# Kernel tuning notes

Hardware: AMD Instinct MI355X
Metric: run time of the kernel (lower is better)

The kernel has to match this reference:

```python
import jax, jax.numpy as jnp
import numpy as np

K = 3          # involution kernel size
GROUPS = 32    # channels == GROUPS * K*K
BN_EPS = 1e-5

def _conv1x1(x, W, b):
    # x: (B,C,H,W), W: (Co,C), b: (Co,)
    return jnp.einsum('bchw,oc->bohw', x, W) + b[None, :, None, None]

def setup_inputs() -> dict:
    key = jax.random.key(0)
    ks = jax.random.split(key, 5)
    C = GROUPS * K * K  # 288
    x = jax.random.normal(ks[0], (8, C, 64, 64), dtype=jnp.float32)
    Wi = jax.random.normal(ks[1], (C, C), dtype=jnp.float32) * 0.05
    bi = jnp.zeros((C,), dtype=jnp.float32)
    gamma = jnp.ones((C,), dtype=jnp.float32)
    beta = jnp.zeros((C,), dtype=jnp.float32)
    Wo = jax.random.normal(ks[2], (C, C), dtype=jnp.float32) * 0.05
    bo = jnp.zeros((C,), dtype=jnp.float32)
    return {"x": x, "Wi": Wi, "bi": bi, "gamma": gamma, "beta": beta, "Wo": Wo, "bo": bo}

def reference(x, Wi, bi, gamma, beta, Wo, bo):
    B, C, H, W = x.shape
    # kernel generation branch (stride=1 -> avgpool is identity)
    tmp = jax.nn.relu(_conv1x1(x, Wi, bi))
    # BatchNorm2d in training mode: batch stats over (N,H,W), biased variance
    mean = jnp.mean(tmp, axis=(0, 2, 3), keepdims=True)
    var = jnp.var(tmp, axis=(0, 2, 3), keepdims=True)
    tmp = (tmp - mean) * jax.lax.rsqrt(var + BN_EPS)
    tmp = tmp * gamma[None, :, None, None] + beta[None, :, None, None]
    ker = _conv1x1(tmp, Wo, bo)                       # (B, G*K^2, H, W)
    ker = ker.reshape(B, GROUPS, K * K, H, W)         # (B, G, K^2, H, W)
    # unfold: extract KxK patches with padding (K-1)//2, stride 1
    p = (K - 1) // 2
    xp = jnp.pad(x, ((0, 0), (0, 0), (p, p), (p, p)))
    patches = jnp.stack(
        [xp[:, :, i:i + H, j:j + W] for i in range(K) for j in range(K)],
        axis=2,
    )  # (B, C, K^2, H, W), kernel-position minor — matches torch unfold layout
    patches = patches.reshape(B, GROUPS, C // GROUPS, K * K, H, W)
    # per-pixel dynamic kernel multiply + sum over kernel positions
    out = jnp.einsum('bgkhw,bgckhw->bgchw', ker, patches)
    return out.reshape(B, C, H, W)
```

## Files before the change

kernel.cpp:

```cpp
#include <hip/hip_runtime.h>

#define CH   288
#define GRPS 32
#define CPG  9
#define IMH  64
#define IMW  64
#define HW   4096
#define NB   8
#define NPX  (NB * HW)
#define BN_EPS 1e-5f

typedef short bf16x8 __attribute__((ext_vector_type(8)));
typedef float f32x4  __attribute__((ext_vector_type(4)));

#define XT_OFF   0u
#define WIB_OFF  18874368u
#define WOS_OFF  19040256u
#define S1_OFF   19206144u
#define S2_OFF   19207296u
#define SC_OFF   19208448u
#define SH_OFF   19209600u
#define BO2_OFF  19210752u

__device__ __forceinline__ unsigned short f2b(float f) {
    unsigned int u = __float_as_uint(f);
    return (unsigned short)((u + 0x7fffu + ((u >> 16) & 1u)) >> 16);
}
__device__ __forceinline__ float b2f(unsigned short h) {
    return __uint_as_float(((unsigned int)h) << 16);
}

#define GLDS(g, l) __builtin_amdgcn_global_load_lds( \
    (const __attribute__((address_space(1))) void*)(g), \
    (__attribute__((address_space(3))) void*)(l), 16, 0, 0)

__device__ __forceinline__ f32x4 mfma16(bf16x8 a, bf16x8 b, f32x4 c) {
    return __builtin_amdgcn_mfma_f32_16x16x32_bf16(a, b, c, 0, 0, 0);
}

#define TS 40
__global__ __launch_bounds__(256) void k_transpose(const float* __restrict__ x,
                                                   unsigned short* __restrict__ xt) {
    __shared__ unsigned short T[64 * TS];
    const int tid = threadIdx.x;
    const int p0 = blockIdx.x * 64;
    const int c0 = blockIdx.y * 32;
    const int b  = blockIdx.z;
    #pragma unroll
    for (int it = 0; it < 2; ++it) {
        const int item  = it * 256 + tid;
        const int c_loc = item >> 4;
        const int p4    = item & 15;
        const float4 v = *(const float4*)(x + (size_t)(b * CH + c0 + c_loc) * HW + p0 + p4 * 4);
        const int px = p4 * 4;
        T[(px + 0) * TS + c_loc] = f2b(v.x);
        T[(px + 1) * TS + c_loc] = f2b(v.y);
        T[(px + 2) * TS + c_loc] = f2b(v.z);
        T[(px + 3) * TS + c_loc] = f2b(v.w);
    }
    __syncthreads();
    const int px_loc = tid >> 2;
    const int cq     = tid & 3;
    const uint4 o = *(const uint4*)((const char*)T + px_loc * (TS * 2) + cq * 16);
    *(uint4*)(xt + ((size_t)b * HW + p0 + px_loc) * CH + c0 + cq * 8) = o;
}

__global__ __launch_bounds__(256) void k_cvt_wi(const float* __restrict__ Wi,
                                                unsigned short* __restrict__ Wib) {
    const int idx = blockIdx.x * 256 + threadIdx.x;
    const float4 v = ((const float4*)Wi)[idx];
    unsigned short h[4] = {f2b(v.x), f2b(v.y), f2b(v.z), f2b(v.w)};
    *(uint2*)(Wib + (size_t)idx * 4) = *(const uint2*)h;
}

__global__ __launch_bounds__(256) void k_gemm1(const unsigned short* __restrict__ Wib,
                                               const float* __restrict__ bi,
                                               unsigned short* __restrict__ xt,
                                               float* __restrict__ s1g) {
    __shared__ unsigned short smem[(64 + 288) * 32];
    char* smc = (char*)smem;

    const int tid  = threadIdx.x;
    const int wave = tid >> 6;
    const int lane = tid & 63;
    const int q    = lane >> 4;
    const int r    = lane & 15;
    const int pxh  = wave & 1;
    const int chh  = wave >> 1;
    const int p0   = blockIdx.x * 64;

    f32x4 acc[2][9];
    #pragma unroll
    for (int t = 0; t < 2; ++t)
        #pragma unroll
        for (int j = 0; j < 9; ++j) acc[t][j] = (f32x4)0.0f;

    const int lrow = lane >> 2;
    const int lp   = lane & 3;

    for (int k0 = 0; k0 < CH; k0 += 32) {
        for (int s = wave; s < 22; s += 4) {
            const int row = s * 16 + lrow;
            const int sc  = lp ^ ((row >> 1) & 3);
            const unsigned short* g = (s < 4)
                ? xt  + (size_t)(p0 + row) * CH + k0 + sc * 8
                : Wib + (size_t)(row - 64) * CH + k0 + sc * 8;
            GLDS(g, smc + s * 1024);
        }
        __syncthreads();
        bf16x8 xf[2];
        #pragma unroll
        for (int t = 0; t < 2; ++t) {
            const int row = pxh * 32 + t * 16 + r;
            xf[t] = *(const bf16x8*)(smc + row * 64 + ((q ^ ((row >> 1) & 3)) * 16));
        }
        #pragma unroll
        for (int j = 0; j < 9; ++j) {
            const int ro = 64 + chh * 144 + j * 16 + r;
            const bf16x8 wf = *(const bf16x8*)(smc + ro * 64 + ((q ^ ((ro >> 1) & 3)) * 16));
            acc[0][j] = mfma16(wf, xf[0], acc[0][j]);
            acc[1][j] = mfma16(wf, xf[1], acc[1][j]);
        }
        __syncthreads();
    }

    float* sstat = (float*)(smc + 18432);
    for (int c2 = tid; c2 < 576; c2 += 256) sstat[c2] = 0.0f;
    __syncthreads();

    #pragma unroll 1
    for (int j = 0; j < 9; ++j) {
        const int cb = chh * 144 + j * 16 + q * 4;
        const float4 b4 = *(const float4*)(bi + cb);
        float a1[4] = {0.f, 0.f, 0.f, 0.f}, a2[4] = {0.f, 0.f, 0.f, 0.f};
        #pragma unroll
        for (int t = 0; t < 2; ++t) {
            float v0 = fmaxf(acc[t][j][0] + b4.x, 0.0f);
            float v1 = fmaxf(acc[t][j][1] + b4.y, 0.0f);
            float v2 = fmaxf(acc[t][j][2] + b4.z, 0.0f);
            float v3 = fmaxf(acc[t][j][3] + b4.w, 0.0f);
            a1[0] += v0; a1[1] += v1; a1[2] += v2; a1[3] += v3;
            a2[0] += v0 * v0; a2[1] += v1 * v1; a2[2] += v2 * v2; a2[3] += v3 * v3;
        }
        #pragma unroll
        for (int m = 1; m < 16; m <<= 1) {
            #pragma unroll
            for (int i = 0; i < 4; ++i) {
                a1[i] += __shfl_xor(a1[i], m, 64);
                a2[i] += __shfl_xor(a2[i], m, 64);
            }
        }
        if (r == 0) {
            #pragma unroll
            for (int i = 0; i < 4; ++i) {
                atomicAdd(&sstat[cb + i], a1[i]);
                atomicAdd(&sstat[288 + cb + i], a2[i]);
            }
        }
    }

    #pragma unroll
    for (int ph = 0; ph < 2; ++ph) {
        const int lr = pxh * 16 + r;
        #pragma unroll
        for (int j = 0; j < 9; ++j) {
            const int cb = chh * 144 + j * 16 + q * 4;
            const float4 b4 = *(const float4*)(bi + cb);
            unsigned short h[4];
            h[0] = f2b(fmaxf(acc[ph][j][0] + b4.x, 0.0f));
            h[1] = f2b(fmaxf(acc[ph][j][1] + b4.y, 0.0f));
            h[2] = f2b(fmaxf(acc[ph][j][2] + b4.z, 0.0f));
            h[3] = f2b(fmaxf(acc[ph][j][3] + b4.w, 0.0f));
            *(uint2*)(smc + lr * 576 + cb * 2) = *(const uint2*)h;
        }
        __syncthreads();
        for (int idx = tid; idx < 1152; idx += 256) {
            const int row = idx / 36;
            const int off = idx - row * 36;
            const int gpx = p0 + ph * 16 + row + (row & 16);
            *(uint4*)(xt + (size_t)gpx * CH + off * 8) =
                *(const uint4*)(smc + row * 576 + off * 16);
        }
        if (ph == 0) {
            for (int c2 = tid; c2 < 576; c2 += 256)
                atomicAdd(&s1g[c2], sstat[c2]);
        }
        __syncthreads();
    }
}

__global__ __launch_bounds__(320) void k_scale(const float* __restrict__ s1,
                                               const float* __restrict__ s2,
                                               const float* __restrict__ gamma,
                                               const float* __restrict__ beta,
                                               float* __restrict__ scale,
                                               float* __restrict__ shift) {
    const int c = threadIdx.x;
    if (c < CH) {
        const float inv = 1.0f / (float)(NB * HW);
        const float mean = s1[c] * inv;
        const float var  = s2[c] * inv - mean * mean;
        const float rs   = rsqrtf(var + BN_EPS);
        const float sc   = gamma[c] * rs;
        scale[c] = sc;
        shift[c] = beta[c] - mean * sc;
    }
}

__global__ __launch_bounds__(64) void k_fold(const float* __restrict__ Wo,
                                             const float* __restrict__ bo,
                                             const float* __restrict__ scale,
                                             const float* __restrict__ shift,
                                             unsigned short* __restrict__ Wos,
                                             float* __restrict__ bo2) {
    const int m = blockIdx.x;
    const int t = threadIdx.x;
    float s = 0.0f;
    for (int k = t; k < CH; k += 64) {
        const float wv = Wo[(size_t)m * CH + k];
        s += wv * shift[k];
        Wos[(size_t)m * CH + k] = f2b(wv * scale[k]);
    }
    #pragma unroll
    for (int off = 32; off > 0; off >>= 1) s += __shfl_down(s, off, 64);
    if (t == 0) bo2[m] = bo[m] + s;
}

#define KLS 36
__global__ __launch_bounds__(256) void k_gemm2_invol(const unsigned short* __restrict__ xt,
                                                     const unsigned short* __restrict__ Wos,
                                                     const float* __restrict__ bo2,
                                                     const float* __restrict__ x,
                                                     float* __restrict__ out) {
    __shared__ unsigned short smem[CH * KLS];
    char* smc = (char*)smem;
    unsigned short* kerL = smem;

    const int tid  = threadIdx.x;
    const int wave = tid >> 6;
    const int lane = tid & 63;
    const int q    = lane >> 4;
    const int r    = lane & 15;
    const int pxh  = wave & 1;
    const int chh  = wave >> 1;
    const int p0   = blockIdx.x * 32;
    const int b    = blockIdx.y;
    const int h    = p0 >> 6;
    const int w0   = p0 & 63;
    const size_t rowbase = (size_t)b * HW + p0;

    f32x4 acc[9];
    #pragma unroll
    for (int j = 0; j < 9; ++j) acc[j] = (f32x4)0.0f;

    const int lrow = lane >> 2;
    const int lp   = lane & 3;

    for (int k0 = 0; k0 < CH; k0 += 32) {
        for (int s = wave; s < 20; s += 4) {
            const int row = s * 16 + lrow;
            const int sc  = lp ^ ((row >> 1) & 3);
            const unsigned short* g = (s < 18)
                ? Wos + (size_t)row * CH + k0 + sc * 8
                : xt  + (rowbase + row - 288) * CH + k0 + sc * 8;
            GLDS(g, smc + s * 1024);
        }
        __syncthreads();
        const int xr = 288 + pxh * 16 + r;
        const bf16x8 xf = *(const bf16x8*)(smc + xr * 64 + ((q ^ ((xr >> 1) & 3)) * 16));
        #pragma unroll
        for (int j = 0; j < 9; ++j) {
            const int wr = chh * 144 + j * 16 + r;
            const bf16x8 wf = *(const bf16x8*)(smc + wr * 64 + ((q ^ ((wr >> 1) & 3)) * 16));
            acc[j] = mfma16(wf, xf, acc[j]);
        }
        __syncthreads();
    }

    const int pxl = pxh * 16 + r;
    #pragma unroll
    for (int j = 0; j < 9; ++j) {
        const int cb = chh * 144 + j * 16 + q * 4;
        const float4 bz = *(const float4*)(bo2 + cb);
        kerL[(cb + 0) * KLS + pxl] = f2b(acc[j][0] + bz.x);
        kerL[(cb + 1) * KLS + pxl] = f2b(acc[j][1] + bz.y);
        kerL[(cb + 2) * KLS + pxl] = f2b(acc[j][2] + bz.z);
        kerL[(cb + 3) * KLS + pxl] = f2b(acc[j][3] + bz.w);
    }
    __syncthreads();

    const int tm = tid >> 3;
    const int tn = tid & 7;
    const int wb = w0 + tn * 4;
    #pragma unroll 1
    for (int i = 0; i < 9; ++i) {
        const int ch = tm + 32 * i;
        const int cb = (ch / CPG) * CPG;
        float xv[3][6];
        #pragma unroll
        for (int dr = 0; dr < 3; ++dr) {
            const int hh = h + dr - 1;
            const bool rv = (hh >= 0) && (hh < IMH);
            const float* xr2 = x + ((size_t)(b * CH + ch) * IMH + (rv ? hh : 0)) * IMW;
            if (rv) {
                const float4 m4 = *(const float4*)(xr2 + wb);
                xv[dr][1] = m4.x; xv[dr][2] = m4.y; xv[dr][3] = m4.z; xv[dr][4] = m4.w;
                xv[dr][0] = (wb > 0)       ? xr2[wb - 1] : 0.0f;
                xv[dr][5] = (wb + 4 < IMW) ? xr2[wb + 4] : 0.0f;
            } else {
                #pragma unroll
                for (int j = 0; j < 6; ++j) xv[dr][j] = 0.0f;
            }
        }
        float o[4] = {0.0f, 0.0f, 0.0f, 0.0f};
        #pragma unroll
        for (int k = 0; k < 9; ++k) {
            const int dr = k / 3, dc = k % 3;
            const uint2 kk = *(const uint2*)(kerL + (cb + k) * KLS + tn * 4);
            const unsigned short* ks = (const unsigned short*)&kk;
            #pragma unroll
            for (int j = 0; j < 4; ++j)
                o[j] += b2f(ks[j]) * xv[dr][j + dc];
        }
        float4 ov = {o[0], o[1], o[2], o[3]};
        *(float4*)(out + ((size_t)(b * CH + ch) * IMH + h) * IMW + wb) = ov;
    }
}

extern "C" void kernel_launch(void* const* d_in, const int* in_sizes, int n_in,
                              void* d_out, int out_size, void* d_ws, size_t ws_size,
                              hipStream_t stream) {
    const float* x     = (const float*)d_in[0];
    const float* Wi    = (const float*)d_in[1];
    const float* bi    = (const float*)d_in[2];
    const float* gamma = (const float*)d_in[3];
    const float* beta  = (const float*)d_in[4];
    const float* Wo    = (const float*)d_in[5];
    const float* bo    = (const float*)d_in[6];
    float* out = (float*)d_out;

    char* ws = (char*)d_ws;
    unsigned short* xt  = (unsigned short*)(ws + XT_OFF);
    unsigned short* Wib = (unsigned short*)(ws + WIB_OFF);
    unsigned short* Wos = (unsigned short*)(ws + WOS_OFF);
    float* s1    = (float*)(ws + S1_OFF);
    float* s2    = (float*)(ws + S2_OFF);
    float* scale = (float*)(ws + SC_OFF);
    float* shift = (float*)(ws + SH_OFF);
    float* bo2   = (float*)(ws + BO2_OFF);

    k_transpose<<<dim3(HW / 64, CH / 32, NB), 256, 0, stream>>>(x, xt);
    k_cvt_wi<<<dim3(CH * CH / 1024), 256, 0, stream>>>(Wi, Wib);
    hipMemsetAsync(ws + S1_OFF, 0, 2 * CH * sizeof(float), stream);
    k_gemm1<<<dim3(NPX / 64), 256, 0, stream>>>(Wib, bi, xt, s1);
    k_scale<<<dim3(1), 320, 0, stream>>>(s1, s2, gamma, beta, scale, shift);
    k_fold<<<dim3(CH), 64, 0, stream>>>(Wo, bo, scale, shift, Wos, bo2);
    k_gemm2_invol<<<dim3(HW / 32, NB), 256, 0, stream>>>(xt, Wos, bo2, x, out);
}
```

Before: 230.2 us.

## Stage three K-slices per barrier and double gemm2 pixel tile to 64

```diff
diff --git a/kernel.cpp b/kernel.cpp
--- a/kernel.cpp
+++ b/kernel.cpp
@@ -37,6 +37,8 @@
 __device__ __forceinline__ f32x4 mfma16(bf16x8 a, bf16x8 b, f32x4 c) {
     return __builtin_amdgcn_mfma_f32_16x16x32_bf16(a, b, c, 0, 0, 0);
 }
+
+#define SUBT 22528
 
 #define TS 40
 __global__ __launch_bounds__(256) void k_transpose(const float* __restrict__ x,
@@ -77,7 +79,7 @@
                                                const float* __restrict__ bi,
                                                unsigned short* __restrict__ xt,
                                                float* __restrict__ s1g) {
-    __shared__ unsigned short smem[(64 + 288) * 32];
+    __shared__ unsigned short smem[3 * 11264];
     char* smc = (char*)smem;
 
     const int tid  = threadIdx.x;
@@ -98,28 +100,36 @@
     const int lrow = lane >> 2;
     const int lp   = lane & 3;
 
-    for (int k0 = 0; k0 < CH; k0 += 32) {
-        for (int s = wave; s < 22; s += 4) {
-            const int row = s * 16 + lrow;
-            const int sc  = lp ^ ((row >> 1) & 3);
-            const unsigned short* g = (s < 4)
-                ? xt  + (size_t)(p0 + row) * CH + k0 + sc * 8
-                : Wib + (size_t)(row - 64) * CH + k0 + sc * 8;
-            GLDS(g, smc + s * 1024);
-        }
-        __syncthreads();
-        bf16x8 xf[2];
-        #pragma unroll
-        for (int t = 0; t < 2; ++t) {
-            const int row = pxh * 32 + t * 16 + r;
-            xf[t] = *(const bf16x8*)(smc + row * 64 + ((q ^ ((row >> 1) & 3)) * 16));
-        }
+    for (int k0 = 0; k0 < CH; k0 += 96) {
+        #pragma unroll
+        for (int kk = 0; kk < 3; ++kk) {
+            for (int s = wave; s < 22; s += 4) {
+                const int row = s * 16 + lrow;
+                const int sc  = lp ^ ((row >> 1) & 3);
+                const unsigned short* g = (s < 4)
+                    ? xt  + (size_t)(p0 + row) * CH + k0 + kk * 32 + sc * 8
+                    : Wib + (size_t)(row - 64) * CH + k0 + kk * 32 + sc * 8;
+                GLDS(g, smc + kk * SUBT + s * 1024);
+            }
+        }
+        __syncthreads();
+        bf16x8 xf[3][2];
+        #pragma unroll
+        for (int kk = 0; kk < 3; ++kk)
+            #pragma unroll
+            for (int t = 0; t < 2; ++t) {
+                const int row = pxh * 32 + t * 16 + r;
+                xf[kk][t] = *(const bf16x8*)(smc + kk * SUBT + row * 64 + ((q ^ ((row >> 1) & 3)) * 16));
+            }
         #pragma unroll
         for (int j = 0; j < 9; ++j) {
             const int ro = 64 + chh * 144 + j * 16 + r;
-            const bf16x8 wf = *(const bf16x8*)(smc + ro * 64 + ((q ^ ((ro >> 1) & 3)) * 16));
-            acc[0][j] = mfma16(wf, xf[0], acc[0][j]);
-            acc[1][j] = mfma16(wf, xf[1], acc[1][j]);
+            #pragma unroll
+            for (int kk = 0; kk < 3; ++kk) {
+                const bf16x8 wf = *(const bf16x8*)(smc + kk * SUBT + ro * 64 + ((q ^ ((ro >> 1) & 3)) * 16));
+                acc[0][j] = mfma16(wf, xf[kk][0], acc[0][j]);
+                acc[1][j] = mfma16(wf, xf[kk][1], acc[1][j]);
+            }
         }
         __syncthreads();
     }
@@ -226,13 +236,13 @@
     if (t == 0) bo2[m] = bo[m] + s;
 }
 
-#define KLS 36
+#define KLS2 68
 __global__ __launch_bounds__(256) void k_gemm2_invol(const unsigned short* __restrict__ xt,
                                                      const unsigned short* __restrict__ Wos,
                                                      const float* __restrict__ bo2,
                                                      const float* __restrict__ x,
                                                      float* __restrict__ out) {
-    __shared__ unsigned short smem[CH * KLS];
+    __shared__ unsigned short smem[3 * 11264];
     char* smc = (char*)smem;
     unsigned short* kerL = smem;
 
@@ -243,58 +253,75 @@
     const int r    = lane & 15;
     const int pxh  = wave & 1;
     const int chh  = wave >> 1;
-    const int p0   = blockIdx.x * 32;
+    const int p0   = blockIdx.x * 64;
     const int b    = blockIdx.y;
-    const int h    = p0 >> 6;
-    const int w0   = p0 & 63;
+    const int h    = blockIdx.x;
     const size_t rowbase = (size_t)b * HW + p0;
 
-    f32x4 acc[9];
-    #pragma unroll
-    for (int j = 0; j < 9; ++j) acc[j] = (f32x4)0.0f;
+    f32x4 acc[2][9];
+    #pragma unroll
+    for (int t = 0; t < 2; ++t)
+        #pragma unroll
+        for (int j = 0; j < 9; ++j) acc[t][j] = (f32x4)0.0f;
 
     const int lrow = lane >> 2;
     const int lp   = lane & 3;
 
-    for (int k0 = 0; k0 < CH; k0 += 32) {
-        for (int s = wave; s < 20; s += 4) {
-            const int row = s * 16 + lrow;
-            const int sc  = lp ^ ((row >> 1) & 3);
-            const unsigned short* g = (s < 18)
-                ? Wos + (size_t)row * CH + k0 + sc * 8
-                : xt  + (rowbase + row - 288) * CH + k0 + sc * 8;
-            GLDS(g, smc + s * 1024);
-        }
-        __syncthreads();
-        const int xr = 288 + pxh * 16 + r;
-        const bf16x8 xf = *(const bf16x8*)(smc + xr * 64 + ((q ^ ((xr >> 1) & 3)) * 16));
+    for (int k0 = 0; k0 < CH; k0 += 96) {
+        #pragma unroll
+        for (int kk = 0; kk < 3; ++kk) {
+            for (int s = wave; s < 22; s += 4) {
+                const int row = s * 16 + lrow;
+                const int sc  = lp ^ ((row >> 1) & 3);
+                const unsigned short* g = (s < 18)
+                    ? Wos + (size_t)row * CH + k0 + kk * 32 + sc * 8
+                    : xt  + (rowbase + row - 288) * CH + k0 + kk * 32 + sc * 8;
+                GLDS(g, smc + kk * SUBT + s * 1024);
+            }
+        }
+        __syncthreads();
+        bf16x8 xf[3][2];
+        #pragma unroll
+        for (int kk = 0; kk < 3; ++kk)
+            #pragma unroll
+            for (int t = 0; t < 2; ++t) {
+                const int xr = 288 + pxh * 32 + t * 16 + r;
+                xf[kk][t] = *(const bf16x8*)(smc + kk * SUBT + xr * 64 + ((q ^ ((xr >> 1) & 3)) * 16));
+            }
         #pragma unroll
         for (int j = 0; j < 9; ++j) {
             const int wr = chh * 144 + j * 16 + r;
-            const bf16x8 wf = *(const bf16x8*)(smc + wr * 64 + ((q ^ ((wr >> 1) & 3)) * 16));
-            acc[j] = mfma16(wf, xf, acc[j]);
-        }
-        __syncthreads();
-    }
-
-    const int pxl = pxh * 16 + r;
+            #pragma unroll
+            for (int kk = 0; kk < 3; ++kk) {
+                const bf16x8 wf = *(const bf16x8*)(smc + kk * SUBT + wr * 64 + ((q ^ ((wr >> 1) & 3)) * 16));
+                acc[0][j] = mfma16(wf, xf[kk][0], acc[0][j]);
+                acc[1][j] = mfma16(wf, xf[kk][1], acc[1][j]);
+            }
+        }
+        __syncthreads();
+    }
+
     #pragma unroll
     for (int j = 0; j < 9; ++j) {
         const int cb = chh * 144 + j * 16 + q * 4;
         const float4 bz = *(const float4*)(bo2 + cb);
-        kerL[(cb + 0) * KLS + pxl] = f2b(acc[j][0] + bz.x);
-        kerL[(cb + 1) * KLS + pxl] = f2b(acc[j][1] + bz.y);
-        kerL[(cb + 2) * KLS + pxl] = f2b(acc[j][2] + bz.z);
-        kerL[(cb + 3) * KLS + pxl] = f2b(acc[j][3] + bz.w);
+        #pragma unroll
+        for (int t = 0; t < 2; ++t) {
+            const int pxl = pxh * 32 + t * 16 + r;
+            kerL[(cb + 0) * KLS2 + pxl] = f2b(acc[t][j][0] + bz.x);
+            kerL[(cb + 1) * KLS2 + pxl] = f2b(acc[t][j][1] + bz.y);
+            kerL[(cb + 2) * KLS2 + pxl] = f2b(acc[t][j][2] + bz.z);
+            kerL[(cb + 3) * KLS2 + pxl] = f2b(acc[t][j][3] + bz.w);
+        }
     }
     __syncthreads();
 
-    const int tm = tid >> 3;
-    const int tn = tid & 7;
-    const int wb = w0 + tn * 4;
+    const int tm = tid >> 4;
+    const int tn = tid & 15;
+    const int wb = tn * 4;
     #pragma unroll 1
-    for (int i = 0; i < 9; ++i) {
-        const int ch = tm + 32 * i;
+    for (int i = 0; i < 18; ++i) {
+        const int ch = tm + 16 * i;
         const int cb = (ch / CPG) * CPG;
         float xv[3][6];
         #pragma unroll
@@ -316,7 +343,7 @@
         #pragma unroll
         for (int k = 0; k < 9; ++k) {
             const int dr = k / 3, dc = k % 3;
-            const uint2 kk = *(const uint2*)(kerL + (cb + k) * KLS + tn * 4);
+            const uint2 kk = *(const uint2*)(kerL + (cb + k) * KLS2 + tn * 4);
             const unsigned short* ks = (const unsigned short*)&kk;
             #pragma unroll
             for (int j = 0; j < 4; ++j)
@@ -355,5 +382,5 @@
     k_gemm1<<<dim3(NPX / 64), 256, 0, stream>>>(Wib, bi, xt, s1);
     k_scale<<<dim3(1), 320, 0, stream>>>(s1, s2, gamma, beta, scale, shift);
     k_fold<<<dim3(CH), 64, 0, stream>>>(Wo, bo, scale, shift, Wos, bo2);
-    k_gemm2_invol<<<dim3(HW / 32, NB), 256, 0, stream>>>(xt, Wos, bo2, x, out);
-}
+    k_gemm2_invol<<<dim3(HW / 64, NB), 256, 0, stream>>>(xt, Wos, bo2, x, out);
+}
```

Result: faster. 191.4 us (-16.8%).

## Double-buffer LDS K-loop with async global-to-LDS prefetch in both GEMMs

Applied to the files above, without the earlier changes.

```diff
diff --git a/kernel.cpp b/kernel.cpp
--- a/kernel.cpp
+++ b/kernel.cpp
@@ -21,6 +21,8 @@
 #define SC_OFF   19208448u
 #define SH_OFF   19209600u
 #define BO2_OFF  19210752u
+
+#define BUFB 20480
 
 __device__ __forceinline__ unsigned short f2b(float f) {
     unsigned int u = __float_as_uint(f);
@@ -73,12 +75,52 @@
     *(uint2*)(Wib + (size_t)idx * 4) = *(const uint2*)h;
 }
 
-__global__ __launch_bounds__(256) void k_gemm1(const unsigned short* __restrict__ Wib,
-                                               const float* __restrict__ bi,
-                                               unsigned short* __restrict__ xt,
-                                               float* __restrict__ s1g) {
-    __shared__ unsigned short smem[(64 + 288) * 32];
-    char* smc = (char*)smem;
+#define STAGE2(XSRC, WSRC, K0v, DST) do {                                      \
+    for (int s = wave; s < 20; s += 4) {                                       \
+        const int row = s * 16 + lrow;                             \
+        const int sc  = lp ^ ((row >> 1) & 3);                                 \
+        const unsigned short* g = (s < 2)                                      \
+            ? (XSRC) + (size_t)row * CH + (K0v) + sc * 8                       \
+            : (WSRC) + (size_t)(row - 32) * CH + (K0v) + sc * 8;               \
+        GLDS(g, (DST) + s * 1024);                                             \
+    }                                                                          \
+} while (0)
+
+#define GSTEP(BUF) do {                                                        \
+    const int xr = pxh * 16 + r;                                               \
+    const bf16x8 xf = *(const bf16x8*)((BUF) + xr * 64 +                       \
+                         ((q ^ ((xr >> 1) & 3)) * 16));                        \
+    _Pragma("unroll")                                                          \
+    for (int j = 0; j < 9; ++j) {                                              \
+        const int wr = 32 + chh * 144 + j * 16 + r;                            \
+        const bf16x8 wf = *(const bf16x8*)((BUF) + wr * 64 +                   \
+                             ((q ^ ((wr >> 1) & 3)) * 16));                    \
+        acc[j] = mfma16(wf, xf, acc[j]);                                       \
+    }                                                                          \
+} while (0)
+
+#define KLOOP(XSRC, WSRC) do {                                                 \
+    STAGE2(XSRC, WSRC, 0, smc);                                                \
+    asm volatile("s_waitcnt vmcnt(0)" ::: "memory");                           \
+    __builtin_amdgcn_s_barrier();                                              \
+    _Pragma("unroll 1")                                                        \
+    for (int kk = 0; kk < 8; ++kk) {                                           \
+        STAGE2(XSRC, WSRC, (kk + 1) * 32, smc + ((kk + 1) & 1) * BUFB);        \
+        asm volatile("s_waitcnt vmcnt(5)" ::: "memory");                       \
+        __builtin_amdgcn_s_barrier();                                          \
+        GSTEP(smc + (kk & 1) * BUFB);                                          \
+        __builtin_amdgcn_s_barrier();                                          \
+    }                                                                          \
+    asm volatile("s_waitcnt vmcnt(0)" ::: "memory");                           \
+    __builtin_amdgcn_s_barrier();                                              \
+    GSTEP(smc);                                                                \
+} while (0)
+
+__global__ __launch_bounds__(256, 4) void k_gemm1(const unsigned short* __restrict__ Wib,
+                                                  const float* __restrict__ bi,
+                                                  unsigned short* __restrict__ xt,
+                                                  float* __restrict__ s1g) {
+    __shared__ char smc[2 * BUFB];
 
     const int tid  = threadIdx.x;
     const int wave = tid >> 6;
@@ -87,44 +129,21 @@
     const int r    = lane & 15;
     const int pxh  = wave & 1;
     const int chh  = wave >> 1;
-    const int p0   = blockIdx.x * 64;
-
-    f32x4 acc[2][9];
-    #pragma unroll
-    for (int t = 0; t < 2; ++t)
-        #pragma unroll
-        for (int j = 0; j < 9; ++j) acc[t][j] = (f32x4)0.0f;
-
-    const int lrow = lane >> 2;
+    const int p0   = blockIdx.x * 32;
+    const int lrow = lane >> 4 == 0 ? lane >> 2 : lane >> 2;
+    const int lrow2 = lane >> 2;
     const int lp   = lane & 3;
-
-    for (int k0 = 0; k0 < CH; k0 += 32) {
-        for (int s = wave; s < 22; s += 4) {
-            const int row = s * 16 + lrow;
-            const int sc  = lp ^ ((row >> 1) & 3);
-            const unsigned short* g = (s < 4)
-                ? xt  + (size_t)(p0 + row) * CH + k0 + sc * 8
-                : Wib + (size_t)(row - 64) * CH + k0 + sc * 8;
-            GLDS(g, smc + s * 1024);
-        }
-        __syncthreads();
-        bf16x8 xf[2];
-        #pragma unroll
-        for (int t = 0; t < 2; ++t) {
-            const int row = pxh * 32 + t * 16 + r;
-            xf[t] = *(const bf16x8*)(smc + row * 64 + ((q ^ ((row >> 1) & 3)) * 16));
-        }
-        #pragma unroll
-        for (int j = 0; j < 9; ++j) {
-            const int ro = 64 + chh * 144 + j * 16 + r;
-            const bf16x8 wf = *(const bf16x8*)(smc + ro * 64 + ((q ^ ((ro >> 1) & 3)) * 16));
-            acc[0][j] = mfma16(wf, xf[0], acc[0][j]);
-            acc[1][j] = mfma16(wf, xf[1], acc[1][j]);
-        }
-        __syncthreads();
-    }
-
-    float* sstat = (float*)(smc + 18432);
+    (void)lrow;
+    #define lrow lrow2
+
+    f32x4 acc[9];
+    #pragma unroll
+    for (int j = 0; j < 9; ++j) acc[j] = (f32x4)0.0f;
+
+    KLOOP(xt + (size_t)p0 * CH, Wib);
+    __syncthreads();
+
+    float* sstat = (float*)(smc + 38656);
     for (int c2 = tid; c2 < 576; c2 += 256) sstat[c2] = 0.0f;
     __syncthreads();
 
@@ -132,16 +151,15 @@
     for (int j = 0; j < 9; ++j) {
         const int cb = chh * 144 + j * 16 + q * 4;
         const float4 b4 = *(const float4*)(bi + cb);
-        float a1[4] = {0.f, 0.f, 0.f, 0.f}, a2[4] = {0.f, 0.f, 0.f, 0.f};
-        #pragma unroll
-        for (int t = 0; t < 2; ++t) {
-            float v0 = fmaxf(acc[t][j][0] + b4.x, 0.0f);
-            float v1 = fmaxf(acc[t][j][1] + b4.y, 0.0f);
-            float v2 = fmaxf(acc[t][j][2] + b4.z, 0.0f);
-            float v3 = fmaxf(acc[t][j][3] + b4.w, 0.0f);
-            a1[0] += v0; a1[1] += v1; a1[2] += v2; a1[3] += v3;
-            a2[0] += v0 * v0; a2[1] += v1 * v1; a2[2] += v2 * v2; a2[3] += v3 * v3;
-        }
+        float v[4];
+        v[0] = fmaxf(acc[j][0] + b4.x, 0.0f);
+        v[1] = fmaxf(acc[j][1] + b4.y, 0.0f);
+        v[2] = fmaxf(acc[j][2] + b4.z, 0.0f);
+        v[3] = fmaxf(acc[j][3] + b4.w, 0.0f);
+        unsigned short h[4] = {f2b(v[0]), f2b(v[1]), f2b(v[2]), f2b(v[3])};
+        *(uint2*)(smc + (pxh * 16 + r) * 576 + cb * 2) = *(const uint2*)h;
+        float a1[4] = {v[0], v[1], v[2], v[3]};
+        float a2[4] = {v[0]*v[0], v[1]*v[1], v[2]*v[2], v[3]*v[3]};
         #pragma unroll
         for (int m = 1; m < 16; m <<= 1) {
             #pragma unroll
@@ -158,35 +176,17 @@
             }
         }
     }
-
-    #pragma unroll
-    for (int ph = 0; ph < 2; ++ph) {
-        const int lr = pxh * 16 + r;
-        #pragma unroll
-        for (int j = 0; j < 9; ++j) {
-            const int cb = chh * 144 + j * 16 + q * 4;
-            const float4 b4 = *(const float4*)(bi + cb);
-            unsigned short h[4];
-            h[0] = f2b(fmaxf(acc[ph][j][0] + b4.x, 0.0f));
-            h[1] = f2b(fmaxf(acc[ph][j][1] + b4.y, 0.0f));
-            h[2] = f2b(fmaxf(acc[ph][j][2] + b4.z, 0.0f));
-            h[3] = f2b(fmaxf(acc[ph][j][3] + b4.w, 0.0f));
-            *(uint2*)(smc + lr * 576 + cb * 2) = *(const uint2*)h;
-        }
-        __syncthreads();
-        for (int idx = tid; idx < 1152; idx += 256) {
-            const int row = idx / 36;
-            const int off = idx - row * 36;
-            const int gpx = p0 + ph * 16 + row + (row & 16);
-            *(uint4*)(xt + (size_t)gpx * CH + off * 8) =
-                *(const uint4*)(smc + row * 576 + off * 16);
-        }
-        if (ph == 0) {
-            for (int c2 = tid; c2 < 576; c2 += 256)
-                atomicAdd(&s1g[c2], sstat[c2]);
-        }
-        __syncthreads();
-    }
+    __syncthreads();
+
+    for (int idx = tid; idx < 1152; idx += 256) {
+        const int row = idx / 36;
+        const int off = idx - row * 36;
+        *(uint4*)(xt + (size_t)(p0 + row) * CH + off * 8) =
+            *(const uint4*)(smc + row * 576 + off * 16);
+    }
+    for (int c2 = tid; c2 < 576; c2 += 256)
+        atomicAdd(&s1g[c2], sstat[c2]);
+    #undef lrow
 }
 
 __global__ __launch_bounds__(320) void k_scale(const float* __restrict__ s1,
@@ -227,14 +227,13 @@
 }
 
 #define KLS 36
-__global__ __launch_bounds__(256) void k_gemm2_invol(const unsigned short* __restrict__ xt,
-                                                     const unsigned short* __restrict__ Wos,
-                                                     const float* __restrict__ bo2,
-                                                     const float* __restrict__ x,
-                                                     float* __restrict__ out) {
-    __shared__ unsigned short smem[CH * KLS];
-    char* smc = (char*)smem;
-    unsigned short* kerL = smem;
+__global__ __launch_bounds__(256, 4) void k_gemm2_invol(const unsigned short* __restrict__ xt,
+                                                        const unsigned short* __restrict__ Wos,
+                                                        const float* __restrict__ bo2,
+                                                        const float* __restrict__ x,
+                                                        float* __restrict__ out) {
+    __shared__ char smc[2 * BUFB];
+    unsigned short* kerL = (unsigned short*)smc;
 
     const int tid  = threadIdx.x;
     const int wave = tid >> 6;
@@ -248,34 +247,15 @@
     const int h    = p0 >> 6;
     const int w0   = p0 & 63;
     const size_t rowbase = (size_t)b * HW + p0;
-
-    f32x4 acc[9];
-    #pragma unroll
-    for (int j = 0; j < 9; ++j) acc[j] = (f32x4)0.0f;
-
     const int lrow = lane >> 2;
     const int lp   = lane & 3;
 
-    for (int k0 = 0; k0 < CH; k0 += 32) {
-        for (int s = wave; s < 20; s += 4) {
-            const int row = s * 16 + lrow;
-            const int sc  = lp ^ ((row >> 1) & 3);
-            const unsigned short* g = (s < 18)
-                ? Wos + (size_t)row * CH + k0 + sc * 8
-                : xt  + (rowbase + row - 288) * CH + k0 + sc * 8;
-            GLDS(g, smc + s * 1024);
-        }
-        __syncthreads();
-        const int xr = 288 + pxh * 16 + r;
-        const bf16x8 xf = *(const bf16x8*)(smc + xr * 64 + ((q ^ ((xr >> 1) & 3)) * 16));
-        #pragma unroll
-        for (int j = 0; j < 9; ++j) {
-            const int wr = chh * 144 + j * 16 + r;
-            const bf16x8 wf = *(const bf16x8*)(smc + wr * 64 + ((q ^ ((wr >> 1) & 3)) * 16));
-            acc[j] = mfma16(wf, xf, acc[j]);
-        }
-        __syncthreads();
-    }
+    f32x4 acc[9];
+    #pragma unroll
+    for (int j = 0; j < 9; ++j) acc[j] = (f32x4)0.0f;
+
+    KLOOP(xt + rowbase * CH, Wos);
+    __syncthreads();
 
     const int pxl = pxh * 16 + r;
     #pragma unroll
@@ -352,7 +332,7 @@
     k_transpose<<<dim3(HW / 64, CH / 32, NB), 256, 0, stream>>>(x, xt);
     k_cvt_wi<<<dim3(CH * CH / 1024), 256, 0, stream>>>(Wi, Wib);
     hipMemsetAsync(ws + S1_OFF, 0, 2 * CH * sizeof(float), stream);
-    k_gemm1<<<dim3(NPX / 64), 256, 0, stream>>>(Wib, bi, xt, s1);
+    k_gemm1<<<dim3(NPX / 32), 256, 0, stream>>>(Wib, bi, xt, s1);
     k_scale<<<dim3(1), 320, 0, stream>>>(s1, s2, gamma, beta, scale, shift);
     k_fold<<<dim3(CH), 64, 0, stream>>>(Wo, bo, scale, shift, Wos, bo2);
     k_gemm2_invol<<<dim3(HW / 32, NB), 256, 0, stream>>>(xt, Wos, bo2, x, out);
```

Result: faster. 204.1 us (-11.3%).
